# Optimization experiments

Hardware: AMD Instinct MI355X
Metric: run time of the kernel (lower is better)

The kernel has to match this reference:

```python
import jax, jax.numpy as jnp
import numpy as np

B, S, T = 32, 64, 64          # batch, src_len, tgt_len
E = 1024                      # embedding_dim
H = 512                       # encoder hidden per direction
H2 = 2 * H                    # decoder hidden = enc_output_dim = 1024
VS, VT = 32000, 32000         # src / tgt vocab
L_ENC, L_DEC = 2, 2


def setup_inputs() -> dict:
    key = jax.random.key(0)
    ks = jax.random.split(key, 16)
    s = 0.05
    return {
        # tokens in [1, V) -> no pad tokens, all src_lens == S
        "x": jax.random.randint(ks[0], (B, S), 1, VS),
        "y": jax.random.randint(ks[1], (B, T), 1, VT),
        "src_emb": jax.random.normal(ks[2], (VS, E), jnp.float32) * s,
        "tgt_emb": jax.random.normal(ks[3], (VT, E), jnp.float32) * s,
        # encoder weights: [layer, dir(0=fwd,1=bwd), 4H, in] with in = E = 2H
        "enc_W_ih": jax.random.normal(ks[4], (L_ENC, 2, 4 * H, E), jnp.float32) * s,
        "enc_W_hh": jax.random.normal(ks[5], (L_ENC, 2, 4 * H, H), jnp.float32) * s,
        "enc_b_ih": jax.random.normal(ks[6], (L_ENC, 2, 4 * H), jnp.float32) * s,
        "enc_b_hh": jax.random.normal(ks[7], (L_ENC, 2, 4 * H), jnp.float32) * s,
        # decoder LSTMCells: cell0 input = E + H2 = 2048, cell1 input = H2
        "dec_W_ih0": jax.random.normal(ks[8], (4 * H2, E + H2), jnp.float32) * s,
        "dec_W_ih1": jax.random.normal(ks[9], (4 * H2, H2), jnp.float32) * s,
        "dec_W_hh": jax.random.normal(ks[10], (L_DEC, 4 * H2, H2), jnp.float32) * s,
        "dec_b_ih": jax.random.normal(ks[11], (L_DEC, 4 * H2), jnp.float32) * s,
        "dec_b_hh": jax.random.normal(ks[12], (L_DEC, 4 * H2), jnp.float32) * s,
        "W_out": jax.random.normal(ks[13], (VT, H2), jnp.float32) * s,
        "b_out": jax.random.normal(ks[14], (VT,), jnp.float32) * s,
    }


def _lstm_cell(x, h, c, W_ih, W_hh, b):
    # PyTorch gate order: i, f, g, o
    gates = x @ W_ih.T + h @ W_hh.T + b
    i, f, g, o = jnp.split(gates, 4, axis=-1)
    c2 = jax.nn.sigmoid(f) * c + jax.nn.sigmoid(i) * jnp.tanh(g)
    h2 = jax.nn.sigmoid(o) * jnp.tanh(c2)
    return h2, c2


def _run_dir(xseq, W_ih, W_hh, b):
    # xseq: [T, B, D] -> outputs [T, B, H], final (h, c)
    Bn, Hn = xseq.shape[1], W_hh.shape[1]
    init = (jnp.zeros((Bn, Hn), xseq.dtype), jnp.zeros((Bn, Hn), xseq.dtype))
    def step(carry, xt):
        h, c = carry
        h2, c2 = _lstm_cell(xt, h, c, W_ih, W_hh, b)
        return (h2, c2), h2
    (hT, cT), ys = jax.lax.scan(step, init, xseq)
    return ys, hT, cT


def _forward(x, y, src_emb, tgt_emb, enc_W_ih, enc_W_hh, enc_b_ih, enc_b_hh,
             dec_W_ih0, dec_W_ih1, dec_W_hh, dec_b_ih, dec_b_hh, W_out, b_out):
    # All src lengths are full -> per-row flip == full flip (pack is a no-op).
    x_rev = jnp.flip(x, axis=1)
    seq = src_emb[x_rev].transpose(1, 0, 2)  # [S, B, E]; dropout=0 (eval)

    h_fin, c_fin = [], []
    for l in range(L_ENC):
        b_f = enc_b_ih[l, 0] + enc_b_hh[l, 0]
        b_b = enc_b_ih[l, 1] + enc_b_hh[l, 1]
        ys_f, hT_f, cT_f = _run_dir(seq, enc_W_ih[l, 0], enc_W_hh[l, 0], b_f)
        ys_b, hT_b, cT_b = _run_dir(seq[::-1], enc_W_ih[l, 1], enc_W_hh[l, 1], b_b)
        seq = jnp.concatenate([ys_f, ys_b[::-1]], axis=-1)  # [S, B, 2H]
        h_fin.append(jnp.concatenate([hT_f, hT_b], axis=-1))  # [B, 2H]
        c_fin.append(jnp.concatenate([cT_f, cT_b], axis=-1))

    context = h_fin[-1]  # cat(hidden[-2], hidden[-1]) = last-layer fwd||bwd

    db0 = dec_b_ih[0] + dec_b_hh[0]
    db1 = dec_b_ih[1] + dec_b_hh[1]
    emb_seq = tgt_emb[y[:, :-1]].transpose(1, 0, 2)  # [T-1, B, E] teacher forcing

    def dec_step(carry, emb_t):
        h0, c0, h1, c1 = carry
        inp0 = jnp.concatenate([emb_t, context], axis=-1)
        h0, c0 = _lstm_cell(inp0, h0, c0, dec_W_ih0, dec_W_hh[0], db0)
        h1, c1 = _lstm_cell(h0, h1, c1, dec_W_ih1, dec_W_hh[1], db1)
        logit = h1 @ W_out.T + b_out
        return (h0, c0, h1, c1), logit

    init = (h_fin[0], c_fin[0], h_fin[1], c_fin[1])
    _, logits = jax.lax.scan(dec_step, init, emb_seq)  # [T-1, B, VT]
    return logits.transpose(1, 0, 2)  # [B, T-1, VT]


def reference(x, y, src_emb, tgt_emb, enc_W_ih, enc_W_hh, enc_b_ih, enc_b_hh,
              dec_W_ih0, dec_W_ih1, dec_W_hh, dec_b_ih, dec_b_hh, W_out, b_out):
    return _forward(x, y, src_emb, tgt_emb, enc_W_ih, enc_W_hh, enc_b_ih, enc_b_hh,
                    dec_W_ih0, dec_W_ih1, dec_W_hh, dec_b_ih, dec_b_hh, W_out, b_out)
```

## Files before the change

### kernel.cpp

```cpp
#include <hip/hip_runtime.h>

typedef __attribute__((ext_vector_type(8))) short short8;
typedef __attribute__((ext_vector_type(4))) float f32x4;

#define DEVINL __device__ __forceinline__

DEVINL unsigned short f2bf(float f) {
  unsigned int u = __builtin_bit_cast(unsigned int, f);
  unsigned int r = u + 0x7FFFu + ((u >> 16) & 1u);
  return (unsigned short)(r >> 16);
}
DEVINL float bf2f(unsigned short u) {
  unsigned int x = ((unsigned int)u) << 16;
  return __builtin_bit_cast(float, x);
}
DEVINL float sig_(float x) { return 1.f / (1.f + __expf(-x)); }
DEVINL float tanh_(float x) { return 2.f / (1.f + __expf(-2.f * x)) - 1.f; }

DEVINL void gld16(void* lds, const void* g) {
  __builtin_amdgcn_global_load_lds(
      (const __attribute__((address_space(1))) unsigned int*)g,
      (__attribute__((address_space(3))) unsigned int*)lds, 16, 0, 0);
}

DEVINL void coh_st(unsigned long long* p, unsigned long long v) {
  __hip_atomic_store(p, v, __ATOMIC_RELAXED, __HIP_MEMORY_SCOPE_AGENT);
}

DEVINL unsigned long long pack4w(unsigned int u, int lane, int s0, int s1) {
  unsigned int p1 = (unsigned int)__shfl_xor((int)u, s0);
  unsigned int lo2 = (lane & s0) ? ((p1 & 0xFFFFu) | (u << 16))
                                 : ((u & 0xFFFFu) | (p1 << 16));
  unsigned int p2 = (unsigned int)__shfl_xor((int)lo2, s1);
  unsigned int lo = (lane & s1) ? p2 : lo2;
  unsigned int hi = (lane & s1) ? lo2 : p2;
  return ((unsigned long long)hi << 32) | lo;
}

DEVINL void bar_arrive(int* arr, int idx, int gen) {
  if (threadIdx.x == 0)
    __hip_atomic_store(arr + idx * 16, gen, __ATOMIC_RELAXED, __HIP_MEMORY_SCOPE_AGENT);
}
DEVINL void wait1(const int* arr, int nb, int gen) {
  if (threadIdx.x < 64) {
    for (;;) {
      int ok = 1;
      for (int i = (int)threadIdx.x; i < nb; i += 64)
        ok &= (__hip_atomic_load(arr + i * 16, __ATOMIC_RELAXED,
                                 __HIP_MEMORY_SCOPE_AGENT) >= gen)
                  ? 1
                  : 0;
      if (__all(ok)) break;
      __builtin_amdgcn_s_sleep(2);
    }
  }
  __builtin_amdgcn_sched_barrier(0);
  asm volatile("" ::: "memory");
  __syncthreads();
}
DEVINL void wait2(const int* a0, int n0, int g0, const int* a1, int n1, int g1) {
  if (threadIdx.x < 64) {
    for (;;) {
      int ok = 1;
      for (int i = (int)threadIdx.x; i < n0; i += 64)
        ok &= (__hip_atomic_load(a0 + i * 16, __ATOMIC_RELAXED,
                                 __HIP_MEMORY_SCOPE_AGENT) >= g0)
                  ? 1
                  : 0;
      for (int i = (int)threadIdx.x; i < n1; i += 64)
        ok &= (__hip_atomic_load(a1 + i * 16, __ATOMIC_RELAXED,
                                 __HIP_MEMORY_SCOPE_AGENT) >= g1)
                  ? 1
                  : 0;
      if (__all(ok)) break;
      __builtin_amdgcn_s_sleep(2);
    }
  }
  __builtin_amdgcn_sched_barrier(0);
  asm volatile("" ::: "memory");
  __syncthreads();
}

__global__ __launch_bounds__(256) void gemm_bf16(
    const unsigned short* __restrict__ A, const unsigned short* __restrict__ Bt,
    void* __restrict__ C, const float* __restrict__ bias,
    int K, int N, int Mvalid, int mode) {
  __shared__ unsigned short lA[1024 * 8];
  __shared__ unsigned short lB[1024 * 8];
  const int tid = threadIdx.x;
  const int lane = tid & 63, wid = tid >> 6;
  const int wm = wid >> 1, wn = wid & 1;
  const int bm = blockIdx.x, bn = blockIdx.y;
  const size_t K_ = (size_t)K;

  const unsigned short* gAc[4];
  const unsigned short* gBc[4];
  unsigned short* lAc[4];
  unsigned short* lBc[4];
#pragma unroll
  for (int c = 0; c < 4; c++) {
    const int s = c * 256 + tid;
    const int r = s & 127, kb = s >> 7;
    gAc[c] = A + (size_t)(bm * 128 + r) * K_ + kb * 8;
    gBc[c] = Bt + (size_t)(bn * 128 + r) * K_ + kb * 8;
    lAc[c] = lA + (size_t)(c * 256 + wid * 64) * 8;
    lBc[c] = lB + (size_t)(c * 256 + wid * 64) * 8;
  }

  f32x4 acc[4][4] = {};
  const int kg = lane >> 4, lr = lane & 15;

  for (int kt = 0; kt < K; kt += 64) {
#pragma unroll
    for (int c = 0; c < 4; c++) {
      gld16(lAc[c], gAc[c] + kt);
      gld16(lBc[c], gBc[c] + kt);
    }
    __syncthreads();
#pragma unroll
    for (int ks = 0; ks < 2; ks++) {
      const int kgi = ks * 4 + kg;
      short8 af[4], bfr[4];
#pragma unroll
      for (int fm = 0; fm < 4; fm++)
        af[fm] = *(const short8*)&lA[(size_t)(kgi * 128 + wm * 64 + fm * 16 + lr) * 8];
#pragma unroll
      for (int fn = 0; fn < 4; fn++)
        bfr[fn] = *(const short8*)&lB[(size_t)(kgi * 128 + wn * 64 + fn * 16 + lr) * 8];
#pragma unroll
      for (int fm = 0; fm < 4; fm++)
#pragma unroll
        for (int fn = 0; fn < 4; fn++)
          acc[fm][fn] =
              __builtin_amdgcn_mfma_f32_16x16x32_bf16(af[fm], bfr[fn], acc[fm][fn], 0, 0, 0);
    }
    __syncthreads();
  }

#pragma unroll
  for (int fn = 0; fn < 4; fn++) {
    const int col = bn * 128 + wn * 64 + fn * 16 + lr;
    const float bv = bias ? bias[col] : 0.f;
#pragma unroll
    for (int fm = 0; fm < 4; fm++) {
      const int row0 = bm * 128 + wm * 64 + fm * 16 + kg * 4;
#pragma unroll
      for (int r = 0; r < 4; r++) {
        const int m = row0 + r;
        if (m < Mvalid) {
          const float v = acc[fm][fn][r] + bv;
          if (mode == 0) {
            ((float*)C)[(size_t)m * N + col] = v;
          } else if (mode == 1) {
            const int b = m & 31, t = m >> 5;
            ((float*)C)[(size_t)b * 2016000 + (size_t)t * 32000 + col] = v;
          } else {
            ((unsigned short*)C)[(size_t)m * N + col] = f2bf(v);
          }
        }
      }
    }
  }
}

__global__ __launch_bounds__(256, 1) void enc_chain(
    const unsigned short* __restrict__ Whh, const unsigned short* __restrict__ G,
    unsigned short* __restrict__ Henc, unsigned short* __restrict__ seq_out,
    float* __restrict__ c_out, int* bar) {
  extern __shared__ unsigned short lw[];
  f32x4* red8 = (f32x4*)((char*)lw + 131072);
  const int tid = threadIdx.x, lane = tid & 63;
  const int lr = lane & 15, kg = lane >> 4;
  const int wv = (tid >> 6) & 1, half = tid >> 7;
  const int dir = (int)blockIdx.x >> 4, j0 = ((int)blockIdx.x & 15) * 32;
  int* arr = bar + dir * 256;
  const int aidx = (int)blockIdx.x & 15;
  const unsigned short* Wd = Whh + (size_t)dir * 2048 * 512;
  for (int it = 0; it < 32; it++) {
    const int idx = (it * 256 + tid) * 16;
    const int r = idx >> 10, o = idx & 1023;
    const unsigned short* src = Wd + (size_t)((r >> 5) * 512 + j0 + (r & 31)) * 512 + (o >> 1);
    *(short8*)((char*)lw + r * 1024 + (o ^ ((r & 7) << 4))) = *(const short8*)src;
  }
  float cc[2][4] = {};
  float gpre[4][2][4];
  auto fetch_g = [&](int t) {
    const int s_idx = dir ? (63 - t) : t;
#pragma unroll
    for (int r = 0; r < 4; r++) {
      const unsigned short* Gr =
          G + (size_t)(s_idx * 32 + (wv * 16 + kg * 4 + r)) * 4096 + dir * 2048;
#pragma unroll
      for (int jh = 0; jh < 2; jh++) {
        const int jj = j0 + jh * 16 + lr;
        gpre[r][jh][0] = bf2f(Gr[jj]);
        gpre[r][jh][1] = bf2f(Gr[512 + jj]);
        gpre[r][jh][2] = bf2f(Gr[1024 + jj]);
        gpre[r][jh][3] = bf2f(Gr[1536 + jj]);
      }
    }
  };
  if (tid < 128) fetch_g(0);
  __syncthreads();
  for (int t = 0; t < 64; t++) {
    const unsigned short* hA =
        Henc + ((size_t)(t * 2 + dir) * 32 + wv * 16 + lr) * 512 + half * 256 + kg * 8;
    short8 areg[8];
#pragma unroll
    for (int kcl = 0; kcl < 8; kcl++) areg[kcl] = *(const short8*)(hA + kcl * 32);
    f32x4 acc[8] = {};
#pragma unroll
    for (int kcl = 0; kcl < 8; kcl++) {
      const int kc = half * 8 + kcl;
#pragma unroll
      for (int nt = 0; nt < 8; nt++) {
        const int rr = nt * 16 + lr;
        short8 bf = *(const short8*)((const char*)lw + rr * 1024 +
                                     ((kc * 64 + kg * 16) ^ ((rr & 7) << 4)));
        acc[nt] = __builtin_amdgcn_mfma_f32_16x16x32_bf16(areg[kcl], bf, acc[nt], 0, 0, 0);
      }
    }
    if (half == 1) {
#pragma unroll
      for (int nt = 0; nt < 8; nt++) red8[nt * 128 + wv * 64 + lane] = acc[nt];
    }
    __syncthreads();
    if (tid < 128) {
      const int s_idx = dir ? (63 - t) : t;
      unsigned long long* HWU =
          (unsigned long long*)Henc + ((size_t)((t + 1) * 2 + dir) * 32) * 128;
#pragma unroll
      for (int nt = 0; nt < 8; nt++) {
        f32x4 ar = red8[nt * 128 + wv * 64 + lane];
        acc[nt][0] += ar[0]; acc[nt][1] += ar[1];
        acc[nt][2] += ar[2]; acc[nt][3] += ar[3];
      }
#pragma unroll
      for (int r = 0; r < 4; r++) {
        const int b = wv * 16 + kg * 4 + r;
#pragma unroll
        for (int jh = 0; jh < 2; jh++) {
          const float gi = gpre[r][jh][0] + acc[jh + 0][r];
          const float gf = gpre[r][jh][1] + acc[jh + 2][r];
          const float gg = gpre[r][jh][2] + acc[jh + 4][r];
          const float go = gpre[r][jh][3] + acc[jh + 6][r];
          const float cn = sig_(gf) * cc[jh][r] + sig_(gi) * tanh_(gg);
          const float hn = sig_(go) * tanh_(cn);
          cc[jh][r] = cn;
          unsigned long long pk = pack4w((unsigned int)f2bf(hn), lane, 1, 2);
          if ((lane & 3) == 0) {
            const int jjb = j0 + jh * 16 + lr;
            coh_st(HWU + b * 128 + (jjb >> 2), pk);
            if (seq_out)
              *(unsigned long long*)&seq_out[(size_t)(s_idx * 32 + b) * 1024 + dir * 512 +
                                             jjb] = pk;
          }
        }
      }
    }
    if (t < 63) {
      __syncthreads();
      bar_arrive(arr, aidx, t + 1);
      if (tid < 128) fetch_g(t + 1);
      wait1(arr, 16, t + 1);
    }
  }
  if (tid < 128) {
#pragma unroll
    for (int r = 0; r < 4; r++)
#pragma unroll
      for (int jh = 0; jh < 2; jh++)
        c_out[(dir * 32 + (wv * 16 + kg * 4 + r)) * 512 + j0 + jh * 16 + lr] = cc[jh][r];
  }
}

__global__ __launch_bounds__(256, 1) void dec_pipe(
    const unsigned short* __restrict__ Whh0, const unsigned short* __restrict__ Wc1,
    const unsigned short* __restrict__ G, const float* __restrict__ db1,
    const float* __restrict__ c0init, const float* __restrict__ c1init,
    unsigned short* __restrict__ H0ext, unsigned short* __restrict__ H1ext,
    int* arr0, int* arr1) {
  extern __shared__ unsigned short lw[];
  f32x4* red4 = (f32x4*)((char*)lw + 131072);
  const int tid = threadIdx.x, lane = tid & 63;
  const int lr = lane & 15, kg = lane >> 4;
  const int wv = (tid >> 6) & 1, half = tid >> 7;
  const int bid = (int)blockIdx.x;

  if (bid < 64) {
    const int j0 = bid * 16, j = j0 + lr;
    for (int it = 0; it < 32; it++) {
      const int idx = (it * 256 + tid) * 16;
      const int r = idx >> 11, o = idx & 2047;
      const unsigned short* src =
          Whh0 + (size_t)((r >> 4) * 1024 + j0 + (r & 15)) * 1024 + (o >> 1);
      *(short8*)((char*)lw + r * 2048 + (o ^ ((r & 7) << 4))) = *(const short8*)src;
    }
    float cc[4] = {};
    float gpre[4][4];
    auto fetch_g = [&](int k) {
#pragma unroll
      for (int r = 0; r < 4; r++) {
        const unsigned short* Gr = G + (size_t)(k * 32 + (wv * 16 + kg * 4 + r)) * 4096 + j;
        gpre[r][0] = bf2f(Gr[0]);
        gpre[r][1] = bf2f(Gr[1024]);
        gpre[r][2] = bf2f(Gr[2048]);
        gpre[r][3] = bf2f(Gr[3072]);
      }
    };
    if (tid < 128) {
#pragma unroll
      for (int r = 0; r < 4; r++) cc[r] = c0init[(wv * 16 + kg * 4 + r) * 1024 + j];
      fetch_g(0);
    }
    __syncthreads();
    for (int k = 0; k < 63; k++) {
      if (k > 0) wait1(arr0, 64, k);
      const unsigned short* hA =
          H0ext + ((size_t)k * 32 + wv * 16 + lr) * 1024 + half * 512 + kg * 8;
      short8 areg[16];
#pragma unroll
      for (int kcl = 0; kcl < 16; kcl++) areg[kcl] = *(const short8*)(hA + kcl * 32);
      f32x4 acc[4] = {};
#pragma unroll
      for (int kcl = 0; kcl < 16; kcl++) {
        const int kc = half * 16 + kcl;
#pragma unroll
        for (int g = 0; g < 4; g++) {
          const int rr = g * 16 + lr;
          short8 bf = *(const short8*)((const char*)lw + rr * 2048 +
                                       ((kc * 64 + kg * 16) ^ ((rr & 7) << 4)));
          acc[g] = __builtin_amdgcn_mfma_f32_16x16x32_bf16(areg[kcl], bf, acc[g], 0, 0, 0);
        }
      }
      if (half == 1) {
#pragma unroll
        for (int g = 0; g < 4; g++) red4[g * 128 + wv * 64 + lane] = acc[g];
      }
      __syncthreads();
      if (tid < 128) {
        unsigned long long* HWU = (unsigned long long*)H0ext + ((size_t)(k + 1) * 32) * 256;
#pragma unroll
        for (int r = 0; r < 4; r++) {
          const int b = wv * 16 + kg * 4 + r;
          f32x4 a0 = red4[0 * 128 + wv * 64 + lane];
          f32x4 a1 = red4[1 * 128 + wv * 64 + lane];
          f32x4 a2 = red4[2 * 128 + wv * 64 + lane];
          f32x4 a3 = red4[3 * 128 + wv * 64 + lane];
          const float gi = gpre[r][0] + acc[0][r] + a0[r];
          const float gf = gpre[r][1] + acc[1][r] + a1[r];
          const float gg = gpre[r][2] + acc[2][r] + a2[r];
          const float go = gpre[r][3] + acc[3][r] + a3[r];
          const float cn = sig_(gf) * cc[r] + sig_(gi) * tanh_(gg);
          const float hn = sig_(go) * tanh_(cn);
          cc[r] = cn;
          unsigned long long pk = pack4w((unsigned int)f2bf(hn), lane, 1, 2);
          if ((lane & 3) == 0)
            coh_st(HWU + b * 256 + ((j0 + lr) >> 2), pk);
        }
      }
      __syncthreads();
      bar_arrive(arr0, bid, k + 1);
      if (tid < 128 && k < 62) fetch_g(k + 1);
    }
  } else {
    const int j0 = (bid - 64) * 8;
    for (int it = 0; it < 32; it++) {
      const int idx = (it * 256 + tid) * 16;
      const int r = idx >> 12, o = idx & 4095;
      const unsigned short* src =
          Wc1 + (size_t)((r & 3) * 1024 + j0 + (r >> 2)) * 2048 + (o >> 1);
      *(short8*)((char*)lw + r * 4096 + (o ^ ((r & 7) << 4))) = *(const short8*)src;
    }
    float cc[2][4] = {};
    float bb1[2][4] = {};
    if (tid < 128) {
#pragma unroll
      for (int n = 0; n < 2; n++) {
        const int j = j0 + n * 4 + (lr >> 2);
#pragma unroll
        for (int g = 0; g < 4; g++) bb1[n][g] = db1[g * 1024 + j];
#pragma unroll
        for (int r = 0; r < 4; r++)
          cc[n][r] = c1init[(wv * 16 + kg * 4 + r) * 1024 + j];
      }
    }
    __syncthreads();
    for (int t = 0; t < 63; t++) {
      wait2(arr0, 64, t + 1, arr1, 128, t);
      const unsigned short* hA =
          half ? (H1ext + ((size_t)t * 32 + wv * 16 + lr) * 1024 + kg * 8)
               : (H0ext + ((size_t)(t + 1) * 32 + wv * 16 + lr) * 1024 + kg * 8);
      short8 areg[32];
#pragma unroll
      for (int kcl = 0; kcl < 32; kcl++) areg[kcl] = *(const short8*)(hA + kcl * 32);
      f32x4 acc[2] = {};
#pragma unroll
      for (int kcl = 0; kcl < 32; kcl++) {
        const int kc = half * 32 + kcl;
#pragma unroll
        for (int n = 0; n < 2; n++) {
          const int rr = n * 16 + lr;
          short8 bf = *(const short8*)((const char*)lw + rr * 4096 +
                                       ((kc * 64 + kg * 16) ^ ((rr & 7) << 4)));
          acc[n] = __builtin_amdgcn_mfma_f32_16x16x32_bf16(areg[kcl], bf, acc[n], 0, 0, 0);
        }
      }
      if (half == 1) {
#pragma unroll
        for (int n = 0; n < 2; n++) red4[n * 128 + wv * 64 + lane] = acc[n];
      }
      __syncthreads();
      if (tid < 128) {
        unsigned long long* HWU = (unsigned long long*)H1ext + ((size_t)(t + 1) * 32) * 256;
#pragma unroll
        for (int n = 0; n < 2; n++) {
          f32x4 ar = red4[n * 128 + wv * 64 + lane];
#pragma unroll
          for (int r = 0; r < 4; r++) {
            const int b = wv * 16 + kg * 4 + r;
            const float v = acc[n][r] + ar[r];
            const float e1a = __shfl_xor(v, 1);
            const float e0 = (lane & 1) ? e1a : v;
            const float e1 = (lane & 1) ? v : e1a;
            const float f0 = __shfl_xor(e0, 2), f1 = __shfl_xor(e1, 2);
            const float gi = ((lane & 2) ? f0 : e0) + bb1[n][0];
            const float gf = ((lane & 2) ? f1 : e1) + bb1[n][1];
            const float gg = ((lane & 2) ? e0 : f0) + bb1[n][2];
            const float go = ((lane & 2) ? e1 : f1) + bb1[n][3];
            const float cn = sig_(gf) * cc[n][r] + sig_(gi) * tanh_(gg);
            const float hn = sig_(go) * tanh_(cn);
            cc[n][r] = cn;
            unsigned long long pk = pack4w((unsigned int)f2bf(hn), lane, 4, 8);
            if ((lane & 15) == 0)
              coh_st(HWU + b * 256 + ((j0 + n * 4) >> 2), pk);
          }
        }
      }
      __syncthreads();
      bar_arrive(arr1, bid - 64, t + 1);
    }
  }
}

struct SetupPtrs {
  const float *encWih, *encWhh, *decWih0, *decWhh, *decWih1, *Wout;
  unsigned short *WihBf, *WhhEncBf, *Wih0Bf, *Whh0Bf, *Wc1Bf, *WoutBf;
  const float *encBa, *encBb;
  float* encBd;
  const float *decBa, *decBb;
  float* decBd;
};

__global__ void setup_all(SetupPtrs p) {
  const long e0 = 2097152, e1 = e0 + 1048576, e2 = e1 + 2097152, e3 = e2 + 1048576;
  const long e4 = e3 + 2097152, e5 = e4 + 8192000, e6 = e5 + 2048, e7 = e6 + 2048;
  const long stride = (long)gridDim.x * blockDim.x;
  for (long i = (long)blockIdx.x * blockDim.x + threadIdx.x; i < e7; i += stride) {
    if (i < e5) {
      const float* s;
      unsigned short* d;
      long k;
      if (i < e0) { s = p.encWih; d = p.WihBf; k = i; }
      else if (i < e1) { s = p.encWhh; d = p.WhhEncBf; k = i - e0; }
      else if (i < e2) { s = p.decWih0; d = p.Wih0Bf; k = i - e1; }
      else if (i < e3) { s = p.decWhh; d = p.Whh0Bf; k = i - e2; }
      else if (i < e4) {
        k = i - e3;
        const long n = k >> 9, c = (k & 511) * 4;
        const float* src = (c < 1024) ? (p.decWih1 + n * 1024 + c)
                                      : (p.decWhh + 4096l * 1024 + n * 1024 + (c - 1024));
        f32x4 v = *(const f32x4*)src;
        ushort4 o = {f2bf(v.x), f2bf(v.y), f2bf(v.z), f2bf(v.w)};
        *(ushort4*)&p.Wc1Bf[k * 4] = o;
        continue;
      } else { s = p.Wout; d = p.WoutBf; k = i - e4; }
      f32x4 v = *(const f32x4*)&s[k * 4];
      ushort4 o = {f2bf(v.x), f2bf(v.y), f2bf(v.z), f2bf(v.w)};
      *(ushort4*)&d[k * 4] = o;
    } else if (i < e6) {
      const long k = i - e5;
      f32x4 a = *(const f32x4*)&p.encBa[k * 4];
      f32x4 b = *(const f32x4*)&p.encBb[k * 4];
      f32x4 o = {a.x + b.x, a.y + b.y, a.z + b.z, a.w + b.w};
      *(f32x4*)&p.encBd[k * 4] = o;
    } else {
      const long k = i - e6;
      f32x4 a = *(const f32x4*)&p.decBa[k * 4];
      f32x4 b = *(const f32x4*)&p.decBb[k * 4];
      f32x4 o = {a.x + b.x, a.y + b.y, a.z + b.z, a.w + b.w};
      *(f32x4*)&p.decBd[k * 4] = o;
    }
  }
}

__global__ void embed_src(const int* __restrict__ x, const float* __restrict__ emb,
                          unsigned short* __restrict__ A0) {
  const int row = blockIdx.x;
  const int s = row >> 5, b = row & 31;
  const int tok = x[b * 64 + (63 - s)];
  const int col = threadIdx.x * 4;
  f32x4 v = *(const f32x4*)(emb + (size_t)tok * 1024 + col);
  ushort4 o = {f2bf(v.x), f2bf(v.y), f2bf(v.z), f2bf(v.w)};
  *(ushort4*)&A0[(size_t)row * 1024 + col] = o;
}

__global__ void embed_tgt(const int* __restrict__ y, const float* __restrict__ emb,
                          unsigned short* __restrict__ inp0) {
  const int row = blockIdx.x;
  const int col = threadIdx.x * 4;
  ushort4 o = {0, 0, 0, 0};
  if (row < 2016) {
    const int t = row >> 5, b = row & 31;
    const int tok = y[b * 64 + t];
    f32x4 v = *(const f32x4*)(emb + (size_t)tok * 1024 + col);
    o = ushort4{f2bf(v.x), f2bf(v.y), f2bf(v.z), f2bf(v.w)};
  } else {
    *(ushort4*)&inp0[(size_t)row * 2048 + 1024 + col] = o;
  }
  *(ushort4*)&inp0[(size_t)row * 2048 + col] = o;
}

__global__ void fill_ctx2(const unsigned short* __restrict__ Hl1,
                          unsigned short* __restrict__ inp0) {
  const int row = blockIdx.x;
  const int b = row & 31;
  const int col = threadIdx.x * 4;
  const int dir = col >> 9, jj = col & 511;
  ushort4 v = *(const ushort4*)(Hl1 + ((size_t)dir * 32 + b) * 512 + jj);
  *(ushort4*)&inp0[(size_t)row * 2048 + 1024 + col] = v;
}

__global__ void dec_init2(const unsigned short* __restrict__ Hl0,
                          const unsigned short* __restrict__ Hl1,
                          const float* __restrict__ Cl0, const float* __restrict__ Cl1,
                          unsigned short* __restrict__ H0e, unsigned short* __restrict__ H1e,
                          float* __restrict__ c0, float* __restrict__ c1) {
  const int i = blockIdx.x * 256 + threadIdx.x;
  const int b = i >> 10, col = i & 1023;
  const int dir = col >> 9, jj = col & 511;
  const int se = (dir * 32 + b) * 512 + jj;
  const int de = b * 1024 + col;
  H0e[de] = Hl0[se];
  H1e[de] = Hl1[se];
  c0[de] = Cl0[se];
  c1[de] = Cl1[se];
}

extern "C" void kernel_launch(void* const* d_in, const int* in_sizes, int n_in,
                              void* d_out, int out_size, void* d_ws, size_t ws_size,
                              hipStream_t stream) {
  const int* x = (const int*)d_in[0];
  const int* y = (const int*)d_in[1];
  const float* src_emb = (const float*)d_in[2];
  const float* tgt_emb = (const float*)d_in[3];
  const float* enc_W_ih = (const float*)d_in[4];
  const float* enc_W_hh = (const float*)d_in[5];
  const float* enc_b_ih = (const float*)d_in[6];
  const float* enc_b_hh = (const float*)d_in[7];
  const float* dec_W_ih0 = (const float*)d_in[8];
  const float* dec_W_ih1 = (const float*)d_in[9];
  const float* dec_W_hh = (const float*)d_in[10];
  const float* dec_b_ih = (const float*)d_in[11];
  const float* dec_b_hh = (const float*)d_in[12];
  const float* W_out = (const float*)d_in[13];
  const float* b_out = (const float*)d_in[14];
  float* out = (float*)d_out;

  char* ws = (char*)d_ws;
  size_t off = 0;
  auto alloc = [&](size_t bytes) -> void* {
    void* p = ws + off;
    off += (bytes + 255) & ~(size_t)255;
    return p;
  };
  unsigned short* A0 = (unsigned short*)alloc(2048ull * 1024 * 2);
  unsigned short* seq1 = (unsigned short*)alloc(2048ull * 1024 * 2);
  unsigned short* Wih_bf = (unsigned short*)alloc(2ull * 4096 * 1024 * 2);
  unsigned short* Wih0_bf = (unsigned short*)alloc(4096ull * 2048 * 2);
  unsigned short* Wout_bf = (unsigned short*)alloc(32000ull * 1024 * 2);
  unsigned short* G = (unsigned short*)alloc(2048ull * 4096 * 2);
  unsigned short* inp0 = (unsigned short*)alloc(2048ull * 2048 * 2);
  unsigned short* Whh_enc_bf = (unsigned short*)alloc(2ull * 2 * 2048 * 512 * 2);
  unsigned short* Whh0_bf = (unsigned short*)alloc(4096ull * 1024 * 2);
  unsigned short* Wc1_bf = (unsigned short*)alloc(4096ull * 2048 * 2);
  unsigned short* H0ext = (unsigned short*)alloc(2080ull * 1024 * 2);
  unsigned short* H1ext = (unsigned short*)alloc(2080ull * 1024 * 2);
  unsigned short* Henc0 = (unsigned short*)alloc(65ull * 2 * 32 * 512 * 2);
  unsigned short* Henc1 = (unsigned short*)alloc(65ull * 2 * 32 * 512 * 2);
  float* encbias = (float*)alloc(2ull * 4096 * 4);
  float* decdb = (float*)alloc(2ull * 4096 * 4);
  float* c_l0 = (float*)alloc(2ull * 32 * 512 * 4);
  float* c_l1 = (float*)alloc(2ull * 32 * 512 * 4);
  float* c0buf = (float*)alloc(32ull * 1024 * 4);
  float* c1buf = (float*)alloc(32ull * 1024 * 4);
  int* bar = (int*)alloc(4096 * 4);
  if (off > ws_size) return;

  (void)hipFuncSetAttribute((const void*)enc_chain,
                            hipFuncAttributeMaxDynamicSharedMemorySize, 147456);
  (void)hipFuncSetAttribute((const void*)dec_pipe,
                            hipFuncAttributeMaxDynamicSharedMemorySize, 139264);

  SetupPtrs sp;
  sp.encWih = enc_W_ih; sp.encWhh = enc_W_hh; sp.decWih0 = dec_W_ih0;
  sp.decWhh = dec_W_hh; sp.decWih1 = dec_W_ih1; sp.Wout = W_out;
  sp.WihBf = Wih_bf; sp.WhhEncBf = Whh_enc_bf; sp.Wih0Bf = Wih0_bf;
  sp.Whh0Bf = Whh0_bf; sp.Wc1Bf = Wc1_bf; sp.WoutBf = Wout_bf;
  sp.encBa = enc_b_ih; sp.encBb = enc_b_hh; sp.encBd = encbias;
  sp.decBa = dec_b_ih; sp.decBb = dec_b_hh; sp.decBd = decdb;
  setup_all<<<2048, 256, 0, stream>>>(sp);
  embed_src<<<2048, 256, 0, stream>>>(x, src_emb, A0);
  embed_tgt<<<2048, 256, 0, stream>>>(y, tgt_emb, inp0);
  hipMemsetAsync(Henc0, 0, 2ull * 32 * 512 * 2, stream);
  hipMemsetAsync(Henc1, 0, 2ull * 32 * 512 * 2, stream);
  hipMemsetAsync(bar, 0, 4096 * 4, stream);

  gemm_bf16<<<dim3(16, 32), 256, 0, stream>>>(A0, Wih_bf, G, encbias, 1024, 4096, 2048, 2);
  enc_chain<<<32, 256, 147456, stream>>>(Whh_enc_bf, G, Henc0, seq1, c_l0, bar + 0);
  gemm_bf16<<<dim3(16, 32), 256, 0, stream>>>(seq1, Wih_bf + 4096ull * 1024, G,
                                              encbias + 4096, 1024, 4096, 2048, 2);
  enc_chain<<<32, 256, 147456, stream>>>(Whh_enc_bf + 2ull * 2048 * 512, G, Henc1, nullptr,
                                         c_l1, bar + 512);

  dec_init2<<<128, 256, 0, stream>>>(Henc0 + 64ull * 2 * 32 * 512,
                                     Henc1 + 64ull * 2 * 32 * 512, c_l0, c_l1,
                                     H0ext, H1ext, c0buf, c1buf);
  fill_ctx2<<<2016, 256, 0, stream>>>(Henc1 + 64ull * 2 * 32 * 512, inp0);
  gemm_bf16<<<dim3(16, 32), 256, 0, stream>>>(inp0, Wih0_bf, G, decdb, 2048, 4096, 2048, 2);

  dec_pipe<<<192, 256, 139264, stream>>>(Whh0_bf, Wc1_bf, G, decdb + 4096, c0buf, c1buf,
                                         H0ext, H1ext, bar + 1024, bar + 2048);

  gemm_bf16<<<dim3(16, 250), 256, 0, stream>>>(H1ext + 32ull * 1024, Wout_bf, out, b_out,
                                               1024, 32000, 2016, 1);
}
```

Measured before the change: 1.968 ms.

## Split decoder recurrent matmul K-dimension across four wave pairs per block

```diff
diff --git a/kernel.cpp b/kernel.cpp
--- a/kernel.cpp
+++ b/kernel.cpp
@@ -274,23 +274,24 @@
   }
 }
 
-__global__ __launch_bounds__(256, 1) void dec_pipe(
+__global__ __launch_bounds__(512, 1) void dec_pipe(
     const unsigned short* __restrict__ Whh0, const unsigned short* __restrict__ Wc1,
     const unsigned short* __restrict__ G, const float* __restrict__ db1,
     const float* __restrict__ c0init, const float* __restrict__ c1init,
     unsigned short* __restrict__ H0ext, unsigned short* __restrict__ H1ext,
     int* arr0, int* arr1) {
   extern __shared__ unsigned short lw[];
-  f32x4* red4 = (f32x4*)((char*)lw + 131072);
+  f32x4* redq = (f32x4*)((char*)lw + 131072);
   const int tid = threadIdx.x, lane = tid & 63;
   const int lr = lane & 15, kg = lane >> 4;
-  const int wv = (tid >> 6) & 1, half = tid >> 7;
+  const int wv = (tid >> 6) & 1, q = tid >> 7;
+  const int t128 = tid & 127;
   const int bid = (int)blockIdx.x;
 
   if (bid < 64) {
     const int j0 = bid * 16, j = j0 + lr;
-    for (int it = 0; it < 32; it++) {
-      const int idx = (it * 256 + tid) * 16;
+    for (int it = 0; it < 16; it++) {
+      const int idx = (it * 512 + tid) * 16;
       const int r = idx >> 11, o = idx & 2047;
       const unsigned short* src =
           Whh0 + (size_t)((r >> 4) * 1024 + j0 + (r & 15)) * 1024 + (o >> 1);
@@ -317,14 +318,14 @@
     for (int k = 0; k < 63; k++) {
       if (k > 0) wait1(arr0, 64, k);
       const unsigned short* hA =
-          H0ext + ((size_t)k * 32 + wv * 16 + lr) * 1024 + half * 512 + kg * 8;
-      short8 areg[16];
-#pragma unroll
-      for (int kcl = 0; kcl < 16; kcl++) areg[kcl] = *(const short8*)(hA + kcl * 32);
+          H0ext + ((size_t)k * 32 + wv * 16 + lr) * 1024 + q * 256 + kg * 8;
+      short8 areg[8];
+#pragma unroll
+      for (int kcl = 0; kcl < 8; kcl++) areg[kcl] = *(const short8*)(hA + kcl * 32);
       f32x4 acc[4] = {};
 #pragma unroll
-      for (int kcl = 0; kcl < 16; kcl++) {
-        const int kc = half * 16 + kcl;
+      for (int kcl = 0; kcl < 8; kcl++) {
+        const int kc = q * 8 + kcl;
 #pragma unroll
         for (int g = 0; g < 4; g++) {
           const int rr = g * 16 + lr;
@@ -333,24 +334,30 @@
           acc[g] = __builtin_amdgcn_mfma_f32_16x16x32_bf16(areg[kcl], bf, acc[g], 0, 0, 0);
         }
       }
-      if (half == 1) {
-#pragma unroll
-        for (int g = 0; g < 4; g++) red4[g * 128 + wv * 64 + lane] = acc[g];
+      if (q > 0) {
+#pragma unroll
+        for (int g = 0; g < 4; g++) redq[(q - 1) * 512 + g * 128 + t128] = acc[g];
       }
       __syncthreads();
       if (tid < 128) {
         unsigned long long* HWU = (unsigned long long*)H0ext + ((size_t)(k + 1) * 32) * 256;
 #pragma unroll
+        for (int g = 0; g < 4; g++) {
+          f32x4 a1 = redq[0 * 512 + g * 128 + t128];
+          f32x4 a2 = redq[1 * 512 + g * 128 + t128];
+          f32x4 a3 = redq[2 * 512 + g * 128 + t128];
+          acc[g][0] += a1[0] + a2[0] + a3[0];
+          acc[g][1] += a1[1] + a2[1] + a3[1];
+          acc[g][2] += a1[2] + a2[2] + a3[2];
+          acc[g][3] += a1[3] + a2[3] + a3[3];
+        }
+#pragma unroll
         for (int r = 0; r < 4; r++) {
           const int b = wv * 16 + kg * 4 + r;
-          f32x4 a0 = red4[0 * 128 + wv * 64 + lane];
-          f32x4 a1 = red4[1 * 128 + wv * 64 + lane];
-          f32x4 a2 = red4[2 * 128 + wv * 64 + lane];
-          f32x4 a3 = red4[3 * 128 + wv * 64 + lane];
-          const float gi = gpre[r][0] + acc[0][r] + a0[r];
-          const float gf = gpre[r][1] + acc[1][r] + a1[r];
-          const float gg = gpre[r][2] + acc[2][r] + a2[r];
-          const float go = gpre[r][3] + acc[3][r] + a3[r];
+          const float gi = gpre[r][0] + acc[0][r];
+          const float gf = gpre[r][1] + acc[1][r];
+          const float gg = gpre[r][2] + acc[2][r];
+          const float go = gpre[r][3] + acc[3][r];
           const float cn = sig_(gf) * cc[r] + sig_(gi) * tanh_(gg);
           const float hn = sig_(go) * tanh_(cn);
           cc[r] = cn;
@@ -365,8 +372,8 @@
     }
   } else {
     const int j0 = (bid - 64) * 8;
-    for (int it = 0; it < 32; it++) {
-      const int idx = (it * 256 + tid) * 16;
+    for (int it = 0; it < 16; it++) {
+      const int idx = (it * 512 + tid) * 16;
       const int r = idx >> 12, o = idx & 4095;
       const unsigned short* src =
           Wc1 + (size_t)((r & 3) * 1024 + j0 + (r >> 2)) * 2048 + (o >> 1);
@@ -389,15 +396,17 @@
     for (int t = 0; t < 63; t++) {
       wait2(arr0, 64, t + 1, arr1, 128, t);
       const unsigned short* hA =
-          half ? (H1ext + ((size_t)t * 32 + wv * 16 + lr) * 1024 + kg * 8)
-               : (H0ext + ((size_t)(t + 1) * 32 + wv * 16 + lr) * 1024 + kg * 8);
-      short8 areg[32];
-#pragma unroll
-      for (int kcl = 0; kcl < 32; kcl++) areg[kcl] = *(const short8*)(hA + kcl * 32);
+          (q < 2)
+              ? (H0ext + ((size_t)(t + 1) * 32 + wv * 16 + lr) * 1024 + (q & 1) * 512 +
+                 kg * 8)
+              : (H1ext + ((size_t)t * 32 + wv * 16 + lr) * 1024 + (q & 1) * 512 + kg * 8);
+      short8 areg[16];
+#pragma unroll
+      for (int kcl = 0; kcl < 16; kcl++) areg[kcl] = *(const short8*)(hA + kcl * 32);
       f32x4 acc[2] = {};
 #pragma unroll
-      for (int kcl = 0; kcl < 32; kcl++) {
-        const int kc = half * 32 + kcl;
+      for (int kcl = 0; kcl < 16; kcl++) {
+        const int kc = q * 16 + kcl;
 #pragma unroll
         for (int n = 0; n < 2; n++) {
           const int rr = n * 16 + lr;
@@ -406,20 +415,22 @@
           acc[n] = __builtin_amdgcn_mfma_f32_16x16x32_bf16(areg[kcl], bf, acc[n], 0, 0, 0);
         }
       }
-      if (half == 1) {
-#pragma unroll
-        for (int n = 0; n < 2; n++) red4[n * 128 + wv * 64 + lane] = acc[n];
+      if (q > 0) {
+#pragma unroll
+        for (int n = 0; n < 2; n++) redq[(q - 1) * 256 + n * 128 + t128] = acc[n];
       }
       __syncthreads();
       if (tid < 128) {
         unsigned long long* HWU = (unsigned long long*)H1ext + ((size_t)(t + 1) * 32) * 256;
 #pragma unroll
         for (int n = 0; n < 2; n++) {
-          f32x4 ar = red4[n * 128 + wv * 64 + lane];
+          f32x4 a1 = redq[0 * 256 + n * 128 + t128];
+          f32x4 a2 = redq[1 * 256 + n * 128 + t128];
+          f32x4 a3 = redq[2 * 256 + n * 128 + t128];
 #pragma unroll
           for (int r = 0; r < 4; r++) {
             const int b = wv * 16 + kg * 4 + r;
-            const float v = acc[n][r] + ar[r];
+            const float v = acc[n][r] + a1[r] + a2[r] + a3[r];
             const float e1a = __shfl_xor(v, 1);
             const float e0 = (lane & 1) ? e1a : v;
             const float e1 = (lane & 1) ? v : e1a;
@@ -600,7 +611,7 @@
   (void)hipFuncSetAttribute((const void*)enc_chain,
                             hipFuncAttributeMaxDynamicSharedMemorySize, 147456);
   (void)hipFuncSetAttribute((const void*)dec_pipe,
-                            hipFuncAttributeMaxDynamicSharedMemorySize, 139264);
+                            hipFuncAttributeMaxDynamicSharedMemorySize, 155648);
 
   SetupPtrs sp;
   sp.encWih = enc_W_ih; sp.encWhh = enc_W_hh; sp.decWih0 = dec_W_ih0;
@@ -629,7 +640,7 @@
   fill_ctx2<<<2016, 256, 0, stream>>>(Henc1 + 64ull * 2 * 32 * 512, inp0);
   gemm_bf16<<<dim3(16, 32), 256, 0, stream>>>(inp0, Wih0_bf, G, decdb, 2048, 4096, 2048, 2);
 
-  dec_pipe<<<192, 256, 139264, stream>>>(Whh0_bf, Wc1_bf, G, decdb + 4096, c0buf, c1buf,
+  dec_pipe<<<192, 512, 155648, stream>>>(Whh0_bf, Wc1_bf, G, decdb + 4096, c0buf, c1buf,
                                          H0ext, H1ext, bar + 1024, bar + 2048);
 
   gemm_bf16<<<dim3(16, 250), 256, 0, stream>>>(H1ext + 32ull * 1024, Wout_bf, out, b_out,
```

New measurement: 1.975 ms. No clear change (+0.3%).
